# Performance work log

Hardware: AMD Instinct MI355X
Metric: run time of the kernel (lower is better)

## Reference

```python
import jax, jax.numpy as jnp
import numpy as np

# Config mirrors CrossAttentionAudio2T(dim=768, n_head=12, num_frames=16, spec_frames=8,
# attn_all_frame=True, audio_patch=196, time_encoding=False, use_stpos=True)
B, T, N, NA, ST, D, H = 4, 8, 196, 196, 8, 768, 12
HD = D // H
SCALE = HD ** -0.5


def setup_inputs() -> dict:
    key = jax.random.key(0)
    ks = jax.random.split(key, 12)
    r = lambda k, s: jax.random.normal(k, s, dtype=jnp.float32)
    return dict(
        t_x=r(ks[0], (B, T * N, D)),
        audio=r(ks[1], (NA + 2, B * ST, D)),
        vmae_space_pos=SCALE * r(ks[2], (N, D)),
        audio_space_pos=SCALE * r(ks[3], (NA, D)),
        vmae_temporal_pos=SCALE * r(ks[4], (T, D)),
        audio_temporal_pos=SCALE * r(ks[5], (ST, D)),
        q_w=0.02 * r(ks[6], (D, D)),
        q_b=jnp.zeros((D,), jnp.float32),
        kv_w=0.02 * r(ks[7], (2 * D, D)),
        kv_b=jnp.zeros((2 * D,), jnp.float32),
        proj_w=0.02 * r(ks[8], (D, D)),
        proj_b=jnp.zeros((D,), jnp.float32),
    )


def reference(t_x, audio, vmae_space_pos, audio_space_pos, vmae_temporal_pos,
              audio_temporal_pos, q_w, q_b, kv_w, kv_b, proj_w, proj_b):
    # --- video query tokens: add spatial + temporal pos embeds ---
    x = t_x.reshape(B, T, N, D) + vmae_space_pos          # [B,T,N,D] + [N,D]
    x = x.transpose(0, 2, 1, 3) + vmae_temporal_pos       # [B,N,T,D] + [T,D]
    x = x.transpose(0, 2, 1, 3).reshape(B, T * N, D)      # 'b n t d -> b (t n) d'

    # --- audio key/value tokens: drop 2 lead tokens, add pos embeds ---
    a = audio[2:].reshape(NA, B, ST, D).transpose(1, 2, 0, 3)  # 'n (b t) d -> b t n d'
    a = a + audio_space_pos                                    # [B,ST,NA,D] + [NA,D]
    a = a.transpose(0, 2, 1, 3) + audio_temporal_pos           # [B,NA,ST,D] + [ST,D]
    a = a.reshape(B, NA * ST, D)                               # 'b n t d -> b (n t) d'

    # --- projections ---
    q = (x @ q_w.T + q_b).reshape(B, T * N, H, HD).transpose(0, 2, 1, 3)   # [B,H,Lq,HD]
    kv = (a @ kv_w.T + kv_b).reshape(B, NA * ST, 2, H, HD)
    k = kv[:, :, 0].transpose(0, 2, 1, 3)                                  # [B,H,Lk,HD]
    v = kv[:, :, 1].transpose(0, 2, 1, 3)

    # --- scaled dot-product cross-attention (full score matrix, as in source) ---
    attn = jax.nn.softmax(jnp.einsum('bhqd,bhkd->bhqk', q * SCALE, k), axis=-1)
    o = jnp.einsum('bhqk,bhkd->bhqd', attn, v)
    o = o.transpose(0, 2, 1, 3).reshape(B, T * N, D)
    return o @ proj_w.T + proj_b
```

## Files before the change

kernel.cpp:

```cpp
#include <hip/hip_runtime.h>

typedef short s8v __attribute__((ext_vector_type(8)));
typedef short s4v __attribute__((ext_vector_type(4)));
typedef float f4v __attribute__((ext_vector_type(4)));

#define LQ 1568
#define LK 1568
#define NH 12
#define LQP 1664

__device__ __forceinline__ unsigned short f2bf(float f) {
  union { float f; unsigned u; } x; x.f = f;
  unsigned r = x.u + 0x7FFFu + ((x.u >> 16) & 1u);
  return (unsigned short)(r >> 16);
}
__device__ __forceinline__ float bf2f(unsigned short s) {
  union { unsigned u; float f; } x; x.u = ((unsigned)s) << 16;
  return x.f;
}

__global__ void prep_all(const float* __restrict__ t_x, const float* __restrict__ audio,
                         const float* __restrict__ sp, const float* __restrict__ asp,
                         const float* __restrict__ tp, const float* __restrict__ atp,
                         const float* __restrict__ q_w, const float* __restrict__ kv_w,
                         const float* __restrict__ proj_w,
                         unsigned short* __restrict__ xb, unsigned short* __restrict__ ab,
                         unsigned short* __restrict__ wq, unsigned short* __restrict__ wkv,
                         unsigned short* __restrict__ wp, int total4) {
  const int n1 = 768 * 768 / 4, n2 = 1536 * 768 / 4;
  const int nconv = 2 * n1 + n2;
  int i = blockIdx.x * 256 + threadIdx.x;
  if (i < nconv) {
    const float* src; unsigned short* dst; int j = i;
    if (i < n1)           { src = q_w;    dst = wq;  }
    else if (i < n1 + n2) { src = kv_w;   dst = wkv; j = i - n1; }
    else                  { src = proj_w; dst = wp;  j = i - n1 - n2; }
    float4 v = *(const float4*)(src + (size_t)j * 4);
    ushort4 o;
    o.x = f2bf(v.x); o.y = f2bf(v.y); o.z = f2bf(v.z); o.w = f2bf(v.w);
    *(ushort4*)(dst + (size_t)j * 4) = o;
    return;
  }
  i -= nconv;
  if (i >= 2 * total4) return;
  if (i < total4) {
    int d4 = (i % 192) * 4;
    int row = i / 192;
    int l = row % LQ;
    int t = l / 196, n = l % 196;
    float4 a  = *(const float4*)(t_x + (size_t)i * 4);
    float4 s  = *(const float4*)(sp + n * 768 + d4);
    float4 tt = *(const float4*)(tp + t * 768 + d4);
    ushort4 o;
    o.x = f2bf(a.x + s.x + tt.x);
    o.y = f2bf(a.y + s.y + tt.y);
    o.z = f2bf(a.z + s.z + tt.z);
    o.w = f2bf(a.w + s.w + tt.w);
    *(ushort4*)(xb + (size_t)i * 4) = o;
  } else {
    i -= total4;
    int d4 = (i % 192) * 4;
    int row = i / 192;
    int b = row / LK;
    int r2 = row % LK;
    int na = r2 >> 3, ta = r2 & 7;
    const float* src = audio + ((size_t)(2 + na) * 32 + b * 8 + ta) * 768 + d4;
    float4 a  = *(const float4*)src;
    float4 s  = *(const float4*)(asp + na * 768 + d4);
    float4 tt = *(const float4*)(atp + ta * 768 + d4);
    ushort4 o;
    o.x = f2bf(a.x + s.x + tt.x);
    o.y = f2bf(a.y + s.y + tt.y);
    o.z = f2bf(a.z + s.z + tt.z);
    o.w = f2bf(a.w + s.w + tt.w);
    *(ushort4*)(ab + (size_t)i * 4) = o;
  }
}

__device__ __forceinline__ void gemm_mainloop(
    const unsigned short* __restrict__ A, const unsigned short* __restrict__ W,
    int K, int row0, int col0,
    unsigned short* As, unsigned short* Bs, f4v acc[4][4]) {
  const int tid = threadIdx.x;
  const int lane = tid & 63, wave = tid >> 6;
  const int wm = wave & 1, wn = wave >> 1;
  const int l15 = lane & 15, quad = lane >> 4;
  const int lr = tid >> 3, lc = (tid & 7) * 8;

  for (int k0 = 0; k0 < K; k0 += 64) {
    __syncthreads();
#pragma unroll
    for (int it = 0; it < 4; ++it) {
      int row = lr + it * 32;
      __builtin_amdgcn_global_load_lds(
          (const __attribute__((address_space(1))) unsigned int*)(A + (size_t)(row0 + row) * K + k0 + lc),
          (__attribute__((address_space(3))) unsigned int*)(As + row * 64 + lc), 16, 0, 0);
      __builtin_amdgcn_global_load_lds(
          (const __attribute__((address_space(1))) unsigned int*)(W + (size_t)(col0 + row) * K + k0 + lc),
          (__attribute__((address_space(3))) unsigned int*)(Bs + row * 64 + lc), 16, 0, 0);
    }
    __syncthreads();
#pragma unroll
    for (int kk = 0; kk < 2; ++kk) {
      s8v af[4], bf[4];
#pragma unroll
      for (int i = 0; i < 4; ++i) {
        af[i] = *(const s8v*)(As + (wm * 64 + i * 16 + l15) * 64 + kk * 32 + quad * 8);
        bf[i] = *(const s8v*)(Bs + (wn * 64 + i * 16 + l15) * 64 + kk * 32 + quad * 8);
      }
#pragma unroll
      for (int mi = 0; mi < 4; ++mi)
#pragma unroll
        for (int ni = 0; ni < 4; ++ni)
          acc[mi][ni] = __builtin_amdgcn_mfma_f32_16x16x32_bf16(af[mi], bf[ni],
                                                               acc[mi][ni], 0, 0, 0);
    }
  }
}

__global__ __launch_bounds__(256, 3) void gemm_qkv(
    const unsigned short* __restrict__ xb, const unsigned short* __restrict__ ab,
    const unsigned short* __restrict__ wq, const unsigned short* __restrict__ wkv,
    const float* __restrict__ q_b, const float* __restrict__ kv_b,
    unsigned short* __restrict__ Qs, unsigned short* __restrict__ Kb,
    unsigned short* __restrict__ Vb) {
  __shared__ __align__(16) unsigned short As[128 * 64];
  __shared__ __align__(16) unsigned short Bs[128 * 64];
  const int tid = threadIdx.x;
  const int lane = tid & 63, wave = tid >> 6;
  const int wm = wave & 1, wn = wave >> 1;
  const int l15 = lane & 15, quad = lane >> 4;
  const int row0 = blockIdx.x * 128;
  const int y = blockIdx.y;
  const bool isQ = (y < 6);
  const int col0 = (isQ ? y : y - 6) * 128;
  const unsigned short* A = isQ ? xb : ab;
  const unsigned short* W = isQ ? wq : wkv;
  const float* bias = isQ ? q_b : kv_b;

  f4v acc[4][4] = {};
  gemm_mainloop(A, W, 768, row0, col0, As, Bs, acc);

#pragma unroll
  for (int mi = 0; mi < 4; ++mi) {
    int rowg = row0 + wm * 64 + mi * 16 + quad * 4;
#pragma unroll
    for (int ni = 0; ni < 4; ++ni) {
      int colg = col0 + wn * 64 + ni * 16 + l15;
      float bv = bias[colg];
      if (!isQ && colg >= 768) {
        int oo = colg - 768;
        int h = oo >> 6, hd = oo & 63;
        int b = rowg / LK, l0 = rowg - b * LK;
        ushort4 pk;
        pk.x = f2bf(acc[mi][ni][0] + bv);
        pk.y = f2bf(acc[mi][ni][1] + bv);
        pk.z = f2bf(acc[mi][ni][2] + bv);
        pk.w = f2bf(acc[mi][ni][3] + bv);
        *(ushort4*)(Vb + ((((size_t)b * NH + h) * 392 + (l0 >> 2)) * 64 + hd) * 4) = pk;
        continue;
      }
#pragma unroll
      for (int r = 0; r < 4; ++r) {
        float v = acc[mi][ni][r] + bv;
        int row = rowg + r;
        int b = row / LQ, l = row - b * LQ;
        int h = colg >> 6, hd = colg & 63;
        if (isQ) {
          v *= 0.18033688011112042f;
          Qs[(((size_t)b * NH + h) * LQ + l) * 64 + hd] = f2bf(v);
        } else {
          Kb[(((size_t)b * NH + h) * LK + l) * 64 + hd] = f2bf(v);
        }
      }
    }
  }
}

__global__ __launch_bounds__(256, 3) void gemm_proj(
    const unsigned short* __restrict__ A, const unsigned short* __restrict__ W,
    const float* __restrict__ bias, float* __restrict__ out) {
  __shared__ __align__(16) unsigned short As[128 * 64];
  __shared__ __align__(16) unsigned short Bs[128 * 64];
  const int tid = threadIdx.x;
  const int lane = tid & 63, wave = tid >> 6;
  const int wm = wave & 1, wn = wave >> 1;
  const int l15 = lane & 15, quad = lane >> 4;
  const int row0 = blockIdx.x * 128;
  const int col0 = blockIdx.y * 128;

  f4v acc[4][4] = {};
  gemm_mainloop(A, W, 768, row0, col0, As, Bs, acc);

#pragma unroll
  for (int mi = 0; mi < 4; ++mi) {
    int rowg = row0 + wm * 64 + mi * 16 + quad * 4;
#pragma unroll
    for (int ni = 0; ni < 4; ++ni) {
      int colg = col0 + wn * 64 + ni * 16 + l15;
      float bv = bias[colg];
#pragma unroll
      for (int r = 0; r < 4; ++r)
        out[(size_t)(rowg + r) * 768 + colg] = acc[mi][ni][r] + bv;
    }
  }
}

__global__ __launch_bounds__(256, 4) void attn(
    const unsigned short* __restrict__ Q, const unsigned short* __restrict__ Kg,
    const unsigned short* __restrict__ Vsw,
    unsigned short* __restrict__ Op, float* __restrict__ Lp) {
  __shared__ __align__(16) unsigned short Kl[112 * 72];
  __shared__ __align__(16) unsigned short Vl[112 * 64];
  const int tid = threadIdx.x;
  const int lane = tid & 63, wave = tid >> 6;
  const int l15 = lane & 15, quad = lane >> 4;
  const int bh = blockIdx.y;
  const int q0 = blockIdx.x * 128;
  const int half = blockIdx.z;
  const int kbeg = half * 784;
  const size_t base = (size_t)bh * LK * 64;

  s8v qf[2][2];
#pragma unroll
  for (int mt = 0; mt < 2; ++mt)
#pragma unroll
    for (int kk = 0; kk < 2; ++kk) {
      int row = q0 + wave * 32 + mt * 16 + l15;
      if (row > LQ - 1) row = LQ - 1;
      qf[mt][kk] = *(const s8v*)(Q + base + (size_t)row * 64 + kk * 32 + quad * 8);
    }

  f4v of[2][4] = {};
  float lr[2] = {0.0f, 0.0f};

  for (int kt = 0; kt < 7; ++kt) {
    int k0 = kbeg + kt * 112;
    __syncthreads();
    for (int c = tid; c < 896; c += 256) {
      int r = c >> 3, kc = c & 7;
      *(uint4*)(Kl + r * 72 + kc * 8) =
          *(const uint4*)(Kg + base + (size_t)(k0 + r) * 64 + kc * 8);
    }
    for (int c = tid; c < 896; c += 256)
      __builtin_amdgcn_global_load_lds(
          (const __attribute__((address_space(1))) unsigned int*)(Vsw + base + (size_t)k0 * 64 + c * 8),
          (__attribute__((address_space(3))) unsigned int*)(Vl + c * 8), 16, 0, 0);
    __syncthreads();

#pragma unroll
    for (int nt = 0; nt < 7; ++nt) {
      s8v kf0 = *(const s8v*)(Kl + (nt * 16 + l15) * 72 + quad * 8);
      s8v kf1 = *(const s8v*)(Kl + (nt * 16 + l15) * 72 + 32 + quad * 8);
      s4v pf[2];
#pragma unroll
      for (int mt = 0; mt < 2; ++mt) {
        f4v s = {};
        s = __builtin_amdgcn_mfma_f32_16x16x32_bf16(kf0, qf[mt][0], s, 0, 0, 0);
        s = __builtin_amdgcn_mfma_f32_16x16x32_bf16(kf1, qf[mt][1], s, 0, 0, 0);
        float p0 = __builtin_amdgcn_exp2f(s[0]);
        float p1 = __builtin_amdgcn_exp2f(s[1]);
        float p2 = __builtin_amdgcn_exp2f(s[2]);
        float p3 = __builtin_amdgcn_exp2f(s[3]);
        lr[mt] += (p0 + p1) + (p2 + p3);
        union { float f; unsigned u; } a0, a1, a2, a3;
        a0.f = p0; a1.f = p1; a2.f = p2; a3.f = p3;
        union { uint2 u; s4v s; } pk;
        pk.u.x = __builtin_amdgcn_perm(a1.u, a0.u, 0x07060302u);
        pk.u.y = __builtin_amdgcn_perm(a3.u, a2.u, 0x07060302u);
        pf[mt] = pk.s;
      }
#pragma unroll
      for (int nd = 0; nd < 4; ++nd) {
        s4v vf = *(const s4v*)(Vl + ((nt * 4 + quad) << 8) + ((nd * 16 + l15) << 2));
        of[0][nd] = __builtin_amdgcn_mfma_f32_16x16x16bf16_1k(pf[0], vf, of[0][nd], 0, 0, 0);
        of[1][nd] = __builtin_amdgcn_mfma_f32_16x16x16bf16_1k(pf[1], vf, of[1][nd], 0, 0, 0);
      }
    }
  }

#pragma unroll
  for (int mt = 0; mt < 2; ++mt) {
    lr[mt] += __shfl_xor(lr[mt], 16);
    lr[mt] += __shfl_xor(lr[mt], 32);
  }

  const size_t obase = ((size_t)(half * 48 + bh) * LQP + q0);
#pragma unroll
  for (int mt = 0; mt < 2; ++mt) {
#pragma unroll
    for (int r = 0; r < 4; ++r) {
      int rowl = wave * 32 + mt * 16 + quad * 4 + r;
#pragma unroll
      for (int nd = 0; nd < 4; ++nd)
        Op[(obase + rowl) * 64 + nd * 16 + l15] = f2bf(of[mt][nd][r]);
    }
    if (quad == 0)
      Lp[obase + wave * 32 + mt * 16 + l15] = lr[mt];
  }
}

__global__ void attn_merge(const unsigned short* __restrict__ Op,
                           const float* __restrict__ Lp,
                           unsigned short* __restrict__ Om) {
  int i = blockIdx.x * 256 + threadIdx.x;
  if (i >= 48 * LQ * 8) return;
  int hd8 = (i & 7) * 8;
  int t = i >> 3;
  int row = t % LQ;
  int bh = t / LQ;
  int b = bh / NH, h = bh - b * NH;
  const unsigned short* p0 = Op + ((size_t)bh * LQP + row) * 64 + hd8;
  const unsigned short* p1 = Op + ((size_t)(48 + bh) * LQP + row) * 64 + hd8;
  float inv = 1.0f / (Lp[(size_t)bh * LQP + row] + Lp[(size_t)(48 + bh) * LQP + row]);
  ushort4 a0 = *(const ushort4*)p0, a1 = *(const ushort4*)(p0 + 4);
  ushort4 b0 = *(const ushort4*)p1, b1 = *(const ushort4*)(p1 + 4);
  ushort4 o0, o1;
  o0.x = f2bf((bf2f(a0.x) + bf2f(b0.x)) * inv);
  o0.y = f2bf((bf2f(a0.y) + bf2f(b0.y)) * inv);
  o0.z = f2bf((bf2f(a0.z) + bf2f(b0.z)) * inv);
  o0.w = f2bf((bf2f(a0.w) + bf2f(b0.w)) * inv);
  o1.x = f2bf((bf2f(a1.x) + bf2f(b1.x)) * inv);
  o1.y = f2bf((bf2f(a1.y) + bf2f(b1.y)) * inv);
  o1.z = f2bf((bf2f(a1.z) + bf2f(b1.z)) * inv);
  o1.w = f2bf((bf2f(a1.w) + bf2f(b1.w)) * inv);
  unsigned short* dst = Om + ((size_t)(b * LQ) + row) * 768 + h * 64 + hd8;
  *(ushort4*)dst = o0;
  *(ushort4*)(dst + 4) = o1;
}

extern "C" void kernel_launch(void* const* d_in, const int* in_sizes, int n_in,
                              void* d_out, int out_size, void* d_ws, size_t ws_size,
                              hipStream_t stream) {
  const float* t_x    = (const float*)d_in[0];
  const float* audio  = (const float*)d_in[1];
  const float* sp     = (const float*)d_in[2];
  const float* asp    = (const float*)d_in[3];
  const float* tp     = (const float*)d_in[4];
  const float* atp    = (const float*)d_in[5];
  const float* q_w    = (const float*)d_in[6];
  const float* q_b    = (const float*)d_in[7];
  const float* kv_w   = (const float*)d_in[8];
  const float* kv_b   = (const float*)d_in[9];
  const float* proj_w = (const float*)d_in[10];
  const float* proj_b = (const float*)d_in[11];
  float* out = (float*)d_out;

  char* ws = (char*)d_ws;
  size_t off = 0;
  auto alloc = [&](size_t bytes) -> void* {
    void* p = ws + off;
    off += (bytes + 255) & ~(size_t)255;
    return p;
  };
  const size_t TOK = 6272;
  unsigned short* xb  = (unsigned short*)alloc(TOK * 768 * 2);
  unsigned short* ab  = (unsigned short*)alloc(TOK * 768 * 2);
  unsigned short* wq  = (unsigned short*)alloc(768 * 768 * 2);
  unsigned short* wkv = (unsigned short*)alloc(1536 * 768 * 2);
  unsigned short* wp  = (unsigned short*)alloc(768 * 768 * 2);
  unsigned short* Qs  = (unsigned short*)alloc(TOK * 768 * 2);
  unsigned short* Kb  = (unsigned short*)alloc(TOK * 768 * 2);
  unsigned short* Vb  = (unsigned short*)alloc(TOK * 768 * 2);

  unsigned short* Op = (unsigned short*)ws;
  float*          Lp = (float*)(ws + (size_t)2 * 48 * LQP * 64 * 2);
  unsigned short* Om = Qs;

  dim3 blk(256);
  const int n1 = 768 * 768 / 4, n2 = 1536 * 768 / 4;
  int total4 = (int)(TOK * 192);
  int nprep = 2 * n1 + n2 + 2 * total4;
  prep_all<<<dim3((nprep + 255) / 256), blk, 0, stream>>>(
      t_x, audio, sp, asp, tp, atp, q_w, kv_w, proj_w, xb, ab, wq, wkv, wp, total4);

  gemm_qkv<<<dim3(49, 18), blk, 0, stream>>>(xb, ab, wq, wkv, q_b, kv_b, Qs, Kb, Vb);

  attn<<<dim3(13, 48, 2), blk, 0, stream>>>(Qs, Kb, Vb, Op, Lp);

  attn_merge<<<dim3((48 * LQ * 8 + 255) / 256), blk, 0, stream>>>(Op, Lp, Om);

  gemm_proj<<<dim3(49, 6), blk, 0, stream>>>(Om, wp, proj_b, out);
}
```

Baseline: 240.9 us.

## Split attention keys into up to 7 chunks and pre-pad K tiles for async LDS loads

```diff
diff --git a/kernel.cpp b/kernel.cpp
--- a/kernel.cpp
+++ b/kernel.cpp
@@ -118,7 +118,7 @@
   }
 }
 
-__global__ __launch_bounds__(256, 3) void gemm_qkv(
+__global__ __launch_bounds__(256, 4) void gemm_qkv(
     const unsigned short* __restrict__ xb, const unsigned short* __restrict__ ab,
     const unsigned short* __restrict__ wq, const unsigned short* __restrict__ wkv,
     const float* __restrict__ q_b, const float* __restrict__ kv_b,
@@ -170,14 +170,15 @@
           v *= 0.18033688011112042f;
           Qs[(((size_t)b * NH + h) * LQ + l) * 64 + hd] = f2bf(v);
         } else {
-          Kb[(((size_t)b * NH + h) * LK + l) * 64 + hd] = f2bf(v);
+          int tile = l / 112, rr = l - tile * 112;
+          Kb[(((size_t)b * NH + h) * 14 + tile) * 8064 + rr * 72 + hd] = f2bf(v);
         }
       }
     }
   }
 }
 
-__global__ __launch_bounds__(256, 3) void gemm_proj(
+__global__ __launch_bounds__(256, 4) void gemm_proj(
     const unsigned short* __restrict__ A, const unsigned short* __restrict__ W,
     const float* __restrict__ bias, float* __restrict__ out) {
   __shared__ __align__(16) unsigned short As[128 * 64];
@@ -209,7 +210,7 @@
 __global__ __launch_bounds__(256, 4) void attn(
     const unsigned short* __restrict__ Q, const unsigned short* __restrict__ Kg,
     const unsigned short* __restrict__ Vsw,
-    unsigned short* __restrict__ Op, float* __restrict__ Lp) {
+    unsigned short* __restrict__ Op, float* __restrict__ Lp, int Z) {
   __shared__ __align__(16) unsigned short Kl[112 * 72];
   __shared__ __align__(16) unsigned short Vl[112 * 64];
   const int tid = threadIdx.x;
@@ -217,8 +218,8 @@
   const int l15 = lane & 15, quad = lane >> 4;
   const int bh = blockIdx.y;
   const int q0 = blockIdx.x * 128;
-  const int half = blockIdx.z;
-  const int kbeg = half * 784;
+  const int z = blockIdx.z;
+  const int t0 = (z * 14) / Z, t1 = ((z + 1) * 14) / Z;
   const size_t base = (size_t)bh * LK * 64;
 
   s8v qf[2][2];
@@ -234,17 +235,17 @@
   f4v of[2][4] = {};
   float lr[2] = {0.0f, 0.0f};
 
-  for (int kt = 0; kt < 7; ++kt) {
-    int k0 = kbeg + kt * 112;
+  for (int kt = t0; kt < t1; ++kt) {
     __syncthreads();
-    for (int c = tid; c < 896; c += 256) {
-      int r = c >> 3, kc = c & 7;
-      *(uint4*)(Kl + r * 72 + kc * 8) =
-          *(const uint4*)(Kg + base + (size_t)(k0 + r) * 64 + kc * 8);
-    }
+    const unsigned short* Ksrc = Kg + ((size_t)bh * 14 + kt) * 8064;
+    for (int c = tid; c < 1008; c += 256)
+      __builtin_amdgcn_global_load_lds(
+          (const __attribute__((address_space(1))) unsigned int*)(Ksrc + c * 8),
+          (__attribute__((address_space(3))) unsigned int*)(Kl + c * 8), 16, 0, 0);
+    const unsigned short* Vsrc = Vsw + base + (size_t)kt * 112 * 64;
     for (int c = tid; c < 896; c += 256)
       __builtin_amdgcn_global_load_lds(
-          (const __attribute__((address_space(1))) unsigned int*)(Vsw + base + (size_t)k0 * 64 + c * 8),
+          (const __attribute__((address_space(1))) unsigned int*)(Vsrc + c * 8),
           (__attribute__((address_space(3))) unsigned int*)(Vl + c * 8), 16, 0, 0);
     __syncthreads();
 
@@ -285,7 +286,7 @@
     lr[mt] += __shfl_xor(lr[mt], 32);
   }
 
-  const size_t obase = ((size_t)(half * 48 + bh) * LQP + q0);
+  const size_t obase = ((size_t)(z * 48 + bh) * LQP + q0);
 #pragma unroll
   for (int mt = 0; mt < 2; ++mt) {
 #pragma unroll
@@ -302,7 +303,7 @@
 
 __global__ void attn_merge(const unsigned short* __restrict__ Op,
                            const float* __restrict__ Lp,
-                           unsigned short* __restrict__ Om) {
+                           unsigned short* __restrict__ Om, int Z) {
   int i = blockIdx.x * 256 + threadIdx.x;
   if (i >= 48 * LQ * 8) return;
   int hd8 = (i & 7) * 8;
@@ -310,20 +311,22 @@
   int row = t % LQ;
   int bh = t / LQ;
   int b = bh / NH, h = bh - b * NH;
-  const unsigned short* p0 = Op + ((size_t)bh * LQP + row) * 64 + hd8;
-  const unsigned short* p1 = Op + ((size_t)(48 + bh) * LQP + row) * 64 + hd8;
-  float inv = 1.0f / (Lp[(size_t)bh * LQP + row] + Lp[(size_t)(48 + bh) * LQP + row]);
-  ushort4 a0 = *(const ushort4*)p0, a1 = *(const ushort4*)(p0 + 4);
-  ushort4 b0 = *(const ushort4*)p1, b1 = *(const ushort4*)(p1 + 4);
+  float acc[8] = {};
+  float lsum = 0.0f;
+  for (int z = 0; z < Z; ++z) {
+    size_t rb = (size_t)(z * 48 + bh) * LQP + row;
+    lsum += Lp[rb];
+    const unsigned short* p = Op + rb * 64 + hd8;
+    ushort4 a0 = *(const ushort4*)p, a1 = *(const ushort4*)(p + 4);
+    acc[0] += bf2f(a0.x); acc[1] += bf2f(a0.y); acc[2] += bf2f(a0.z); acc[3] += bf2f(a0.w);
+    acc[4] += bf2f(a1.x); acc[5] += bf2f(a1.y); acc[6] += bf2f(a1.z); acc[7] += bf2f(a1.w);
+  }
+  float inv = 1.0f / lsum;
   ushort4 o0, o1;
-  o0.x = f2bf((bf2f(a0.x) + bf2f(b0.x)) * inv);
-  o0.y = f2bf((bf2f(a0.y) + bf2f(b0.y)) * inv);
-  o0.z = f2bf((bf2f(a0.z) + bf2f(b0.z)) * inv);
-  o0.w = f2bf((bf2f(a0.w) + bf2f(b0.w)) * inv);
-  o1.x = f2bf((bf2f(a1.x) + bf2f(b1.x)) * inv);
-  o1.y = f2bf((bf2f(a1.y) + bf2f(b1.y)) * inv);
-  o1.z = f2bf((bf2f(a1.z) + bf2f(b1.z)) * inv);
-  o1.w = f2bf((bf2f(a1.w) + bf2f(b1.w)) * inv);
+  o0.x = f2bf(acc[0] * inv); o0.y = f2bf(acc[1] * inv);
+  o0.z = f2bf(acc[2] * inv); o0.w = f2bf(acc[3] * inv);
+  o1.x = f2bf(acc[4] * inv); o1.y = f2bf(acc[5] * inv);
+  o1.z = f2bf(acc[6] * inv); o1.w = f2bf(acc[7] * inv);
   unsigned short* dst = Om + ((size_t)(b * LQ) + row) * 768 + h * 64 + hd8;
   *(ushort4*)dst = o0;
   *(ushort4*)(dst + 4) = o1;
@@ -360,11 +363,28 @@
   unsigned short* wkv = (unsigned short*)alloc(1536 * 768 * 2);
   unsigned short* wp  = (unsigned short*)alloc(768 * 768 * 2);
   unsigned short* Qs  = (unsigned short*)alloc(TOK * 768 * 2);
-  unsigned short* Kb  = (unsigned short*)alloc(TOK * 768 * 2);
+  unsigned short* Kb  = (unsigned short*)alloc((size_t)48 * 14 * 8064 * 2);
   unsigned short* Vb  = (unsigned short*)alloc(TOK * 768 * 2);
 
-  unsigned short* Op = (unsigned short*)ws;
-  float*          Lp = (float*)(ws + (size_t)2 * 48 * LQP * 64 * 2);
+  auto need = [&](int Z) {
+    return off + (size_t)Z * 48 * LQP * 64 * 2 + (size_t)Z * 48 * LQP * 4 + 512;
+  };
+  int Z;
+  unsigned short* Op;
+  float* Lp;
+  if (ws_size >= need(7)) {
+    Z = 7;
+    Op = (unsigned short*)alloc((size_t)7 * 48 * LQP * 64 * 2);
+    Lp = (float*)alloc((size_t)7 * 48 * LQP * 4);
+  } else if (ws_size >= need(4)) {
+    Z = 4;
+    Op = (unsigned short*)alloc((size_t)4 * 48 * LQP * 64 * 2);
+    Lp = (float*)alloc((size_t)4 * 48 * LQP * 4);
+  } else {
+    Z = 2;
+    Op = (unsigned short*)ws;
+    Lp = (float*)(ws + (size_t)2 * 48 * LQP * 64 * 2);
+  }
   unsigned short* Om = Qs;
 
   dim3 blk(256);
@@ -376,9 +396,9 @@
 
   gemm_qkv<<<dim3(49, 18), blk, 0, stream>>>(xb, ab, wq, wkv, q_b, kv_b, Qs, Kb, Vb);
 
-  attn<<<dim3(13, 48, 2), blk, 0, stream>>>(Qs, Kb, Vb, Op, Lp);
-
-  attn_merge<<<dim3((48 * LQ * 8 + 255) / 256), blk, 0, stream>>>(Op, Lp, Om);
+  attn<<<dim3(13, 48, Z), blk, 0, stream>>>(Qs, Kb, Vb, Op, Lp, Z);
+
+  attn_merge<<<dim3((48 * LQ * 8 + 255) / 256), blk, 0, stream>>>(Op, Lp, Om, Z);
 
   gemm_proj<<<dim3(49, 6), blk, 0, stream>>>(Om, wp, proj_b, out);
 }
```

Result: no change. 236.3 us (-1.9%).
